# Performance work log

Hardware: AMD Instinct MI355X
Metric: run time of the kernel (lower is better)

Reference implementation:

```python
import jax, jax.numpy as jnp
import numpy as np

E, H, F, T = 8, 2048, 4096, 16384  # experts, hidden, ffn, total tokens


def setup_inputs() -> dict:
    key = jax.random.key(0)
    k1, k2, k3 = jax.random.split(key, 3)
    std = 1.0 / np.sqrt(H)
    x = jax.random.normal(k1, (T, H), dtype=jnp.float32)
    # trunc_normal_(std=std) ~ normal * std for reference purposes
    w_gate_up = jax.random.normal(k2, (E, 2 * F, H), dtype=jnp.float32) * std
    w_down = jax.random.normal(k3, (E, H, F), dtype=jnp.float32) * std
    # tokens are pre-sorted by expert; uniform routing: T//E tokens per expert
    tokens_per_expert = jnp.full((E,), T // E, dtype=jnp.int64)
    return {"x": x, "w_gate_up": w_gate_up, "w_down": w_down,
            "tokens_per_expert": tokens_per_expert}


def reference(x, w_gate_up, w_down, tokens_per_expert):
    # x: [T, H] sorted by expert; uniform tokens_per_expert => grouped GEMM
    # is a batched GEMM over the expert axis (same math as the per-expert
    # sequential fallback: gate_up = xi @ w_gate_up[i].T, etc.).
    e = w_gate_up.shape[0]
    f = w_down.shape[2]
    xe = x.reshape(e, -1, x.shape[-1])                     # [E, T/E, H]
    gate_up = jnp.einsum('eth,efh->etf', xe, w_gate_up)    # [E, T/E, 2F]
    gate, up = gate_up[..., :f], gate_up[..., f:]
    hidden = jax.nn.silu(gate) * up                        # [E, T/E, F]
    out = jnp.einsum('etf,ehf->eth', hidden, w_down)       # [E, T/E, H]
    return out.reshape(x.shape)
```

## Files before the change

kernel.cpp:

```cpp
#include <hip/hip_runtime.h>
#include <stdint.h>

typedef unsigned short u16;
typedef unsigned int u32;
typedef short bf16x8 __attribute__((ext_vector_type(8)));
typedef float f32x4 __attribute__((ext_vector_type(4)));

#define E_ 8
#define H_ 2048
#define F_ 4096
#define T_ 16384
#define TE_ 2048

#define WAITV(n) asm volatile("s_waitcnt vmcnt(" #n ")" ::: "memory")
#define BARF                       \
  do {                             \
    asm volatile("" ::: "memory"); \
    __builtin_amdgcn_s_barrier();  \
    asm volatile("" ::: "memory"); \
  } while (0)

__device__ __forceinline__ u16 f2bf(float f) {
  u32 u = __builtin_bit_cast(u32, f);
  u32 r = (u + 0x7FFFu + ((u >> 16) & 1u)) >> 16;
  return (u16)r;
}

__device__ __forceinline__ void gload16(const u16* g, u16* l) {
  __builtin_amdgcn_global_load_lds(
      (__attribute__((address_space(1))) void*)g,
      (__attribute__((address_space(3))) void*)l, 16, 0, 0);
}

__device__ __forceinline__ void mfma_b(f32x4& acc, bf16x8 a, bf16x8 b) {
  asm volatile("v_mfma_f32_16x16x32_bf16 %0, %1, %2, %0"
               : "+v"(acc)
               : "v"(a), "v"(b));
}


__global__ __launch_bounds__(256) void cvt_kernel(const float* __restrict__ src,
                                                  u16* __restrict__ dst,
                                                  long n4) {
  long i = (long)blockIdx.x * blockDim.x + threadIdx.x;
  long stride = (long)gridDim.x * blockDim.x;
  const float4* s4 = (const float4*)src;
  uint2* d4 = (uint2*)dst;
  for (; i < n4; i += stride) {
    float4 v = s4[i];
    uint2 o;
    o.x = (u32)f2bf(v.x) | ((u32)f2bf(v.y) << 16);
    o.y = (u32)f2bf(v.z) | ((u32)f2bf(v.w) << 16);
    d4[i] = o;
  }
}


__global__ __launch_bounds__(256, 2) void gemm1_silu(
    const u16* __restrict__ Xb, const u16* __restrict__ Wgu,
    u16* __restrict__ Hid, long sX, long sW, long sH) {
  const int z = blockIdx.z;
  Xb += (long)z * sX;
  Wgu += (long)z * sW;
  Hid += (long)z * sH;

  const int bx = blockIdx.x;
  const int by = blockIdx.y;
  const int tid = threadIdx.x;
  const int w = tid >> 6;
  const int lane = tid & 63;
  const int wr = w >> 1, wc = w & 1;
  const int fr = lane & 15, q = lane >> 4, l7 = lane & 7;

  __shared__ __attribute__((aligned(16))) u16 lds[2 * 16384];

  const int srow8 = lane >> 3;
  const int sgran = (lane & 7) ^ (lane >> 3);
  const u16* gA = Xb + (size_t)(by * 128 + srow8) * H_ + sgran * 8;
  const u16* gBg = Wgu + (size_t)(bx * 64 + srow8) * H_ + sgran * 8;
  const u16* gBu = gBg + (size_t)F_ * H_;

  auto stage = [&](int t, int buf) {
    u16* L = lds + buf * 16384;
    const int ko = t * 64;
#pragma unroll
    for (int i = 0; i < 4; ++i) {
      const int c = i * 4 + w;
      gload16(gA + (size_t)(c * 8) * H_ + ko, L + c * 512 + lane * 8);
    }
#pragma unroll
    for (int i = 0; i < 2; ++i) {
      const int c = i * 4 + w;
      gload16(gBg + (size_t)(c * 8) * H_ + ko, L + 8192 + c * 512 + lane * 8);
      gload16(gBu + (size_t)(c * 8) * H_ + ko, L + 12288 + c * 512 + lane * 8);
    }
  };

  f32x4 accG[4][2] = {};
  f32x4 accU[4][2] = {};

  auto comp = [&](int buf) {
    const u16* L = lds + buf * 16384;
#pragma unroll
    for (int ks = 0; ks < 2; ++ks) {
      const int seg = (((ks << 2) + q) ^ l7) << 3;
      bf16x8 a[4], bg[2], bu[2];
#pragma unroll
      for (int mi = 0; mi < 4; ++mi)
        a[mi] = *(const bf16x8*)&L[(wr * 64 + mi * 16 + fr) * 64 + seg];
#pragma unroll
      for (int ni = 0; ni < 2; ++ni) {
        bg[ni] = *(const bf16x8*)&L[8192 + (wc * 32 + ni * 16 + fr) * 64 + seg];
        bu[ni] =
            *(const bf16x8*)&L[12288 + (wc * 32 + ni * 16 + fr) * 64 + seg];
      }
      __builtin_amdgcn_s_setprio(1);
#pragma unroll
      for (int mi = 0; mi < 4; ++mi)
#pragma unroll
        for (int ni = 0; ni < 2; ++ni) {
          mfma_b(accG[mi][ni], a[mi], bg[ni]);
          mfma_b(accU[mi][ni], a[mi], bu[ni]);
        }
      __builtin_amdgcn_s_setprio(0);
    }
  };

  const int NT = H_ / 64;
  stage(0, 0);
  stage(1, 1);
  for (int t = 0; t < NT - 1; ++t) {
    WAITV(8);
    BARF;
    comp(t & 1);
    BARF;
    if (t + 2 < NT) stage(t + 2, t & 1);
  }
  WAITV(0);
  BARF;
  comp((NT - 1) & 1);

  const int row0 = by * 128 + wr * 64 + q * 4;
  const int col0 = bx * 64 + wc * 32 + fr;
#pragma unroll
  for (int mi = 0; mi < 4; ++mi)
#pragma unroll
    for (int ni = 0; ni < 2; ++ni)
#pragma unroll
      for (int j = 0; j < 4; ++j) {
        float g = accG[mi][ni][j];
        float u = accU[mi][ni][j];
        float h = (g / (1.f + __expf(-g))) * u;
        Hid[(size_t)(row0 + mi * 16 + j) * F_ + col0 + ni * 16] = f2bf(h);
      }
}


__global__ __launch_bounds__(256, 2) void gemm2_down(
    const u16* __restrict__ Hd, const u16* __restrict__ Wd,
    float* __restrict__ Out, long sH, long sW, long sO) {
  const int z = blockIdx.z;
  Hd += (long)z * sH;
  Wd += (long)z * sW;
  Out += (long)z * sO;

  const int bx = blockIdx.x;
  const int by = blockIdx.y;
  const int tid = threadIdx.x;
  const int w = tid >> 6;
  const int lane = tid & 63;
  const int wr = w >> 1, wc = w & 1;
  const int fr = lane & 15, q = lane >> 4, l7 = lane & 7;

  __shared__ __attribute__((aligned(16))) u16 lds[2 * 16384];

  const int srow8 = lane >> 3;
  const int sgran = (lane & 7) ^ (lane >> 3);
  const u16* gA = Hd + (size_t)(by * 128 + srow8) * F_ + sgran * 8;
  const u16* gB = Wd + (size_t)(bx * 128 + srow8) * F_ + sgran * 8;

  auto stage = [&](int t, int buf) {
    u16* L = lds + buf * 16384;
    const int ko = t * 64;
#pragma unroll
    for (int i = 0; i < 4; ++i) {
      const int c = i * 4 + w;
      gload16(gA + (size_t)(c * 8) * F_ + ko, L + c * 512 + lane * 8);
      gload16(gB + (size_t)(c * 8) * F_ + ko, L + 8192 + c * 512 + lane * 8);
    }
  };

  f32x4 acc[4][4] = {};

  auto comp = [&](int buf) {
    const u16* L = lds + buf * 16384;
#pragma unroll
    for (int ks = 0; ks < 2; ++ks) {
      const int seg = (((ks << 2) + q) ^ l7) << 3;
      bf16x8 a[4], b[4];
#pragma unroll
      for (int mi = 0; mi < 4; ++mi)
        a[mi] = *(const bf16x8*)&L[(wr * 64 + mi * 16 + fr) * 64 + seg];
#pragma unroll
      for (int ni = 0; ni < 4; ++ni)
        b[ni] = *(const bf16x8*)&L[8192 + (wc * 64 + ni * 16 + fr) * 64 + seg];
      __builtin_amdgcn_s_setprio(1);
#pragma unroll
      for (int mi = 0; mi < 4; ++mi)
#pragma unroll
        for (int ni = 0; ni < 4; ++ni) mfma_b(acc[mi][ni], a[mi], b[ni]);
      __builtin_amdgcn_s_setprio(0);
    }
  };

  const int NT = F_ / 64;
  stage(0, 0);
  stage(1, 1);
  for (int t = 0; t < NT - 1; ++t) {
    WAITV(8);
    BARF;
    comp(t & 1);
    BARF;
    if (t + 2 < NT) stage(t + 2, t & 1);
  }
  WAITV(0);
  BARF;
  comp((NT - 1) & 1);

  const int row0 = by * 128 + wr * 64 + q * 4;
  const int col0 = bx * 128 + wc * 64 + fr;
#pragma unroll
  for (int mi = 0; mi < 4; ++mi)
#pragma unroll
    for (int ni = 0; ni < 4; ++ni)
#pragma unroll
      for (int j = 0; j < 4; ++j)
        Out[(size_t)(row0 + mi * 16 + j) * H_ + col0 + ni * 16] =
            acc[mi][ni][j];
}


extern "C" void kernel_launch(void* const* d_in, const int* in_sizes, int n_in,
                              void* d_out, int out_size, void* d_ws,
                              size_t ws_size, hipStream_t stream) {
  (void)in_sizes;
  (void)n_in;
  (void)out_size;
  const float* x = (const float*)d_in[0];
  const float* wgu = (const float*)d_in[1];
  const float* wdn = (const float*)d_in[2];
  float* out = (float*)d_out;
  u16* ws = (u16*)d_ws;

  const size_t xbN = (size_t)T_ * H_;
  const size_t wguN = (size_t)E_ * 2 * F_ * H_;
  const size_t wdnN = (size_t)E_ * H_ * F_;
  const size_t hidN = (size_t)T_ * F_;
  const size_t fullBytes = (xbN + wguN + wdnN + hidN) * 2;

  dim3 cblk(256), gblk(256);

  if (ws_size >= fullBytes) {
    u16* xb = ws;
    u16* wgub = xb + xbN;
    u16* wdnb = wgub + wguN;
    u16* hid = wdnb + wdnN;
    cvt_kernel<<<2048, cblk, 0, stream>>>(x, xb, (long)(xbN / 4));
    cvt_kernel<<<4096, cblk, 0, stream>>>(wgu, wgub, (long)(wguN / 4));
    cvt_kernel<<<4096, cblk, 0, stream>>>(wdn, wdnb, (long)(wdnN / 4));
    gemm1_silu<<<dim3(F_ / 64, TE_ / 128, E_), gblk, 0, stream>>>(
        xb, wgub, hid, (long)TE_ * H_, (long)2 * F_ * H_, (long)TE_ * F_);
    gemm2_down<<<dim3(H_ / 128, TE_ / 128, E_), gblk, 0, stream>>>(
        hid, wdnb, out, (long)TE_ * F_, (long)H_ * F_, (long)TE_ * H_);
  } else {
    u16* xb = ws;
    u16* wgub = xb + (size_t)TE_ * H_;
    u16* wdnb = wgub + (size_t)2 * F_ * H_;
    u16* hid = wdnb + (size_t)H_ * F_;
    for (int e = 0; e < E_; ++e) {
      cvt_kernel<<<1024, cblk, 0, stream>>>(x + (size_t)e * TE_ * H_, xb,
                                            (long)((size_t)TE_ * H_ / 4));
      cvt_kernel<<<2048, cblk, 0, stream>>>(wgu + (size_t)e * 2 * F_ * H_, wgub,
                                            (long)((size_t)2 * F_ * H_ / 4));
      cvt_kernel<<<2048, cblk, 0, stream>>>(wdn + (size_t)e * H_ * F_, wdnb,
                                            (long)((size_t)H_ * F_ / 4));
      gemm1_silu<<<dim3(F_ / 64, TE_ / 128, 1), gblk, 0, stream>>>(xb, wgub,
                                                                   hid, 0, 0,
                                                                   0);
      gemm2_down<<<dim3(H_ / 128, TE_ / 128, 1), gblk, 0, stream>>>(
          hid, wdnb, out + (size_t)e * TE_ * H_, 0, 0, 0);
    }
  }
}
```

Before: 1.075 ms.

## Merge x/w_gate_up conversions and overlap w_down conversion with gemm1

Replaces the two separate fp32-to-bf16 conversion launches for x and w_gate_up with one launch that splits its blocks between the two arrays. It also adds an extra column of blocks to the gemm1 grid that converts w_down while the GEMM blocks run, which removes the standalone w_down conversion launch. The aim is to cut launch overhead and tail gaps and to hide the w_down conversion behind gemm1's compute. The risk is that the conversion blocks compete with the GEMM for bandwidth and CU slots. In the fallback path the conversion blocks are indexed only by blockIdx.y, so the fixed 131072-element chunk size must match each expert's w_down slice for the conversion to be complete and stay in bounds.

Result: slower. 1.286 ms (+19.6%).

```diff
diff --git a/kernel.cpp b/kernel.cpp
--- a/kernel.cpp
+++ b/kernel.cpp
@@ -38,33 +38,55 @@
                : "v"(a), "v"(b));
 }
 
-
-__global__ __launch_bounds__(256) void cvt_kernel(const float* __restrict__ src,
-                                                  u16* __restrict__ dst,
-                                                  long n4) {
-  long i = (long)blockIdx.x * blockDim.x + threadIdx.x;
-  long stride = (long)gridDim.x * blockDim.x;
-  const float4* s4 = (const float4*)src;
-  uint2* d4 = (uint2*)dst;
-  for (; i < n4; i += stride) {
-    float4 v = s4[i];
-    uint2 o;
-    o.x = (u32)f2bf(v.x) | ((u32)f2bf(v.y) << 16);
-    o.y = (u32)f2bf(v.z) | ((u32)f2bf(v.w) << 16);
-    d4[i] = o;
+__device__ __forceinline__ void cvt_f4(const float4* __restrict__ s4,
+                                       uint2* __restrict__ d4, long i) {
+  float4 v = s4[i];
+  uint2 o;
+  o.x = (u32)f2bf(v.x) | ((u32)f2bf(v.y) << 16);
+  o.y = (u32)f2bf(v.z) | ((u32)f2bf(v.w) << 16);
+  d4[i] = o;
+}
+
+
+__global__ __launch_bounds__(256) void cvt2_kernel(
+    const float* __restrict__ s0, u16* __restrict__ d0, long n0,
+    const float* __restrict__ s1, u16* __restrict__ d1, long n1, int b0) {
+  if ((int)blockIdx.x < b0) {
+    long i = (long)blockIdx.x * blockDim.x + threadIdx.x;
+    long stride = (long)b0 * blockDim.x;
+    const float4* s4 = (const float4*)s0;
+    uint2* d4 = (uint2*)d0;
+    for (; i < n0; i += stride) cvt_f4(s4, d4, i);
+  } else {
+    long i = (long)(blockIdx.x - b0) * blockDim.x + threadIdx.x;
+    long stride = (long)(gridDim.x - b0) * blockDim.x;
+    const float4* s4 = (const float4*)s1;
+    uint2* d4 = (uint2*)d1;
+    for (; i < n1; i += stride) cvt_f4(s4, d4, i);
   }
 }
 
 
 __global__ __launch_bounds__(256, 2) void gemm1_silu(
     const u16* __restrict__ Xb, const u16* __restrict__ Wgu,
-    u16* __restrict__ Hid, long sX, long sW, long sH) {
+    u16* __restrict__ Hid, const float* __restrict__ WdnSrc,
+    u16* __restrict__ WdnDst, long sX, long sW, long sH) {
+  const int bx = blockIdx.x;
+  if (bx == (int)gridDim.x - 1) {
+    const long cid = (long)blockIdx.z * gridDim.y + blockIdx.y;
+    const long base = cid * 131072;
+    const float4* s4 = (const float4*)WdnSrc;
+    uint2* d4 = (uint2*)WdnDst;
+    for (long i = base + threadIdx.x; i < base + 131072; i += 256)
+      cvt_f4(s4, d4, i);
+    return;
+  }
+
   const int z = blockIdx.z;
   Xb += (long)z * sX;
   Wgu += (long)z * sW;
   Hid += (long)z * sH;
 
-  const int bx = blockIdx.x;
   const int by = blockIdx.y;
   const int tid = threadIdx.x;
   const int w = tid >> 6;
@@ -265,11 +287,11 @@
     u16* wgub = xb + xbN;
     u16* wdnb = wgub + wguN;
     u16* hid = wdnb + wdnN;
-    cvt_kernel<<<2048, cblk, 0, stream>>>(x, xb, (long)(xbN / 4));
-    cvt_kernel<<<4096, cblk, 0, stream>>>(wgu, wgub, (long)(wguN / 4));
-    cvt_kernel<<<4096, cblk, 0, stream>>>(wdn, wdnb, (long)(wdnN / 4));
-    gemm1_silu<<<dim3(F_ / 64, TE_ / 128, E_), gblk, 0, stream>>>(
-        xb, wgub, hid, (long)TE_ * H_, (long)2 * F_ * H_, (long)TE_ * F_);
+    cvt2_kernel<<<4096, cblk, 0, stream>>>(x, xb, (long)(xbN / 4), wgu, wgub,
+                                           (long)(wguN / 4), 832);
+    gemm1_silu<<<dim3(F_ / 64 + 1, TE_ / 128, E_), gblk, 0, stream>>>(
+        xb, wgub, hid, wdn, wdnb, (long)TE_ * H_, (long)2 * F_ * H_,
+        (long)TE_ * F_);
     gemm2_down<<<dim3(H_ / 128, TE_ / 128, E_), gblk, 0, stream>>>(
         hid, wdnb, out, (long)TE_ * F_, (long)H_ * F_, (long)TE_ * H_);
   } else {
@@ -278,15 +300,12 @@
     u16* wdnb = wgub + (size_t)2 * F_ * H_;
     u16* hid = wdnb + (size_t)H_ * F_;
     for (int e = 0; e < E_; ++e) {
-      cvt_kernel<<<1024, cblk, 0, stream>>>(x + (size_t)e * TE_ * H_, xb,
-                                            (long)((size_t)TE_ * H_ / 4));
-      cvt_kernel<<<2048, cblk, 0, stream>>>(wgu + (size_t)e * 2 * F_ * H_, wgub,
-                                            (long)((size_t)2 * F_ * H_ / 4));
-      cvt_kernel<<<2048, cblk, 0, stream>>>(wdn + (size_t)e * H_ * F_, wdnb,
-                                            (long)((size_t)H_ * F_ / 4));
-      gemm1_silu<<<dim3(F_ / 64, TE_ / 128, 1), gblk, 0, stream>>>(xb, wgub,
-                                                                   hid, 0, 0,
-                                                                   0);
+      cvt2_kernel<<<2048, cblk, 0, stream>>>(
+          x + (size_t)e * TE_ * H_, xb, (long)((size_t)TE_ * H_ / 4),
+          wgu + (size_t)e * 2 * F_ * H_, wgub,
+          (long)((size_t)2 * F_ * H_ / 4), 410);
+      gemm1_silu<<<dim3(F_ / 64 + 1, TE_ / 128, 1), gblk, 0, stream>>>(
+          xb, wgub, hid, wdn + (size_t)e * H_ * F_, wdnb, 0, 0, 0);
       gemm2_down<<<dim3(H_ / 128, TE_ / 128, 1), gblk, 0, stream>>>(
           hid, wdnb, out + (size_t)e * TE_ * H_, 0, 0, 0);
     }
```

## Fuse fp32 weight-to-bf16 conversion into GEMM B-tile staging

Applied to the files above, without the earlier changes.

Removes the standalone weight conversion kernels. The GEMMs now load fp32 weights into registers, convert them with packed bf16 conversion instructions and store them to LDS, using a register-staged double-buffer pipeline. This cuts a full extra read/write pass over the large weight tensors. In exchange, each block re-reads twice as many bytes for its weight tiles and uses more registers for staging, which may lower occupancy.

New measurement: 1.331 ms. 23.8% more time.

```diff
diff --git a/kernel.cpp b/kernel.cpp
--- a/kernel.cpp
+++ b/kernel.cpp
@@ -13,6 +13,7 @@
 #define TE_ 2048
 
 #define WAITV(n) asm volatile("s_waitcnt vmcnt(" #n ")" ::: "memory")
+#define LGKM0 asm volatile("s_waitcnt lgkmcnt(0)" ::: "memory")
 #define BARF                       \
   do {                             \
     asm volatile("" ::: "memory"); \
@@ -24,6 +25,12 @@
   u32 u = __builtin_bit_cast(u32, f);
   u32 r = (u + 0x7FFFu + ((u >> 16) & 1u)) >> 16;
   return (u16)r;
+}
+
+__device__ __forceinline__ u32 cvtpk(float lo, float hi) {
+  u32 r;
+  asm("v_cvt_pk_bf16_f32 %0, %1, %2" : "=v"(r) : "v"(lo), "v"(hi));
+  return r;
 }
 
 __device__ __forceinline__ void gload16(const u16* g, u16* l) {
@@ -57,7 +64,7 @@
 
 
 __global__ __launch_bounds__(256, 2) void gemm1_silu(
-    const u16* __restrict__ Xb, const u16* __restrict__ Wgu,
+    const u16* __restrict__ Xb, const float* __restrict__ Wgu,
     u16* __restrict__ Hid, long sX, long sW, long sH) {
   const int z = blockIdx.z;
   Xb += (long)z * sX;
@@ -77,10 +84,10 @@
   const int srow8 = lane >> 3;
   const int sgran = (lane & 7) ^ (lane >> 3);
   const u16* gA = Xb + (size_t)(by * 128 + srow8) * H_ + sgran * 8;
-  const u16* gBg = Wgu + (size_t)(bx * 64 + srow8) * H_ + sgran * 8;
-  const u16* gBu = gBg + (size_t)F_ * H_;
-
-  auto stage = [&](int t, int buf) {
+  const float4* gB4 =
+      (const float4*)Wgu + (size_t)(bx * 64 + srow8) * (H_ / 4) + sgran * 2;
+
+  auto stageA = [&](int t, int buf) {
     u16* L = lds + buf * 16384;
     const int ko = t * 64;
 #pragma unroll
@@ -88,11 +95,32 @@
       const int c = i * 4 + w;
       gload16(gA + (size_t)(c * 8) * H_ + ko, L + c * 512 + lane * 8);
     }
-#pragma unroll
-    for (int i = 0; i < 2; ++i) {
-      const int c = i * 4 + w;
-      gload16(gBg + (size_t)(c * 8) * H_ + ko, L + 8192 + c * 512 + lane * 8);
-      gload16(gBu + (size_t)(c * 8) * H_ + ko, L + 12288 + c * 512 + lane * 8);
+  };
+
+  auto loadB = [&](float4* r, int t) {
+    const size_t kt = (size_t)t * 16;
+#pragma unroll
+    for (int i = 0; i < 4; ++i) {
+      const int c = i * 4 + w;
+      const size_t roff = (i < 2) ? (size_t)c * 8 * (H_ / 4)
+                                  : (size_t)F_ * (H_ / 4) +
+                                        (size_t)(c - 8) * 8 * (H_ / 4);
+      r[2 * i] = gB4[roff + kt];
+      r[2 * i + 1] = gB4[roff + kt + 1];
+    }
+  };
+
+  auto writeB = [&](int buf, const float4* r) {
+    u16* L = lds + buf * 16384;
+#pragma unroll
+    for (int i = 0; i < 4; ++i) {
+      const int c = i * 4 + w;
+      uint4 v;
+      v.x = cvtpk(r[2 * i].x, r[2 * i].y);
+      v.y = cvtpk(r[2 * i].z, r[2 * i].w);
+      v.z = cvtpk(r[2 * i + 1].x, r[2 * i + 1].y);
+      v.w = cvtpk(r[2 * i + 1].z, r[2 * i + 1].w);
+      *(uint4*)&L[8192 + c * 512 + lane * 8] = v;
     }
   };
 
@@ -126,19 +154,45 @@
     }
   };
 
+  float4 rB0[8], rB1[8];
   const int NT = H_ / 64;
-  stage(0, 0);
-  stage(1, 1);
-  for (int t = 0; t < NT - 1; ++t) {
-    WAITV(8);
-    BARF;
-    comp(t & 1);
-    BARF;
-    if (t + 2 < NT) stage(t + 2, t & 1);
+  loadB(rB0, 0);
+  stageA(0, 0);
+  loadB(rB1, 1);
+  stageA(1, 1);
+  WAITV(16);
+  writeB(0, rB0);
+  WAITV(12);
+  LGKM0;
+  BARF;
+  for (int t = 0; t < NT - 2; t += 2) {
+    comp(0);
+    BARF;
+    loadB(rB0, t + 2);
+    stageA(t + 2, 0);
+    WAITV(16);
+    writeB(1, rB1);
+    WAITV(12);
+    LGKM0;
+    BARF;
+    comp(1);
+    BARF;
+    loadB(rB1, t + 3);
+    stageA(t + 3, 1);
+    WAITV(16);
+    writeB(0, rB0);
+    WAITV(12);
+    LGKM0;
+    BARF;
   }
+  comp(0);
+  BARF;
+  WAITV(4);
+  writeB(1, rB1);
   WAITV(0);
-  BARF;
-  comp((NT - 1) & 1);
+  LGKM0;
+  BARF;
+  comp(1);
 
   const int row0 = by * 128 + wr * 64 + q * 4;
   const int col0 = bx * 64 + wc * 32 + fr;
@@ -157,7 +211,7 @@
 
 
 __global__ __launch_bounds__(256, 2) void gemm2_down(
-    const u16* __restrict__ Hd, const u16* __restrict__ Wd,
+    const u16* __restrict__ Hd, const float* __restrict__ Wd,
     float* __restrict__ Out, long sH, long sW, long sO) {
   const int z = blockIdx.z;
   Hd += (long)z * sH;
@@ -177,16 +231,41 @@
   const int srow8 = lane >> 3;
   const int sgran = (lane & 7) ^ (lane >> 3);
   const u16* gA = Hd + (size_t)(by * 128 + srow8) * F_ + sgran * 8;
-  const u16* gB = Wd + (size_t)(bx * 128 + srow8) * F_ + sgran * 8;
-
-  auto stage = [&](int t, int buf) {
+  const float4* gB4 =
+      (const float4*)Wd + (size_t)(bx * 128 + srow8) * (F_ / 4) + sgran * 2;
+
+  auto stageA = [&](int t, int buf) {
     u16* L = lds + buf * 16384;
     const int ko = t * 64;
 #pragma unroll
     for (int i = 0; i < 4; ++i) {
       const int c = i * 4 + w;
       gload16(gA + (size_t)(c * 8) * F_ + ko, L + c * 512 + lane * 8);
-      gload16(gB + (size_t)(c * 8) * F_ + ko, L + 8192 + c * 512 + lane * 8);
+    }
+  };
+
+  auto loadB = [&](float4* r, int t) {
+    const size_t kt = (size_t)t * 16;
+#pragma unroll
+    for (int i = 0; i < 4; ++i) {
+      const int c = i * 4 + w;
+      const size_t roff = (size_t)c * 8 * (F_ / 4);
+      r[2 * i] = gB4[roff + kt];
+      r[2 * i + 1] = gB4[roff + kt + 1];
+    }
+  };
+
+  auto writeB = [&](int buf, const float4* r) {
+    u16* L = lds + buf * 16384;
+#pragma unroll
+    for (int i = 0; i < 4; ++i) {
+      const int c = i * 4 + w;
+      uint4 v;
+      v.x = cvtpk(r[2 * i].x, r[2 * i].y);
+      v.y = cvtpk(r[2 * i].z, r[2 * i].w);
+      v.z = cvtpk(r[2 * i + 1].x, r[2 * i + 1].y);
+      v.w = cvtpk(r[2 * i + 1].z, r[2 * i + 1].w);
+      *(uint4*)&L[8192 + c * 512 + lane * 8] = v;
     }
   };
 
@@ -213,19 +292,45 @@
     }
   };
 
+  float4 rB0[8], rB1[8];
   const int NT = F_ / 64;
-  stage(0, 0);
-  stage(1, 1);
-  for (int t = 0; t < NT - 1; ++t) {
-    WAITV(8);
-    BARF;
-    comp(t & 1);
-    BARF;
-    if (t + 2 < NT) stage(t + 2, t & 1);
+  loadB(rB0, 0);
+  stageA(0, 0);
+  loadB(rB1, 1);
+  stageA(1, 1);
+  WAITV(16);
+  writeB(0, rB0);
+  WAITV(12);
+  LGKM0;
+  BARF;
+  for (int t = 0; t < NT - 2; t += 2) {
+    comp(0);
+    BARF;
+    loadB(rB0, t + 2);
+    stageA(t + 2, 0);
+    WAITV(16);
+    writeB(1, rB1);
+    WAITV(12);
+    LGKM0;
+    BARF;
+    comp(1);
+    BARF;
+    loadB(rB1, t + 3);
+    stageA(t + 3, 1);
+    WAITV(16);
+    writeB(0, rB0);
+    WAITV(12);
+    LGKM0;
+    BARF;
   }
+  comp(0);
+  BARF;
+  WAITV(4);
+  writeB(1, rB1);
   WAITV(0);
-  BARF;
-  comp((NT - 1) & 1);
+  LGKM0;
+  BARF;
+  comp(1);
 
   const int row0 = by * 128 + wr * 64 + q * 4;
   const int col0 = bx * 128 + wc * 64 + fr;
@@ -253,42 +358,29 @@
   u16* ws = (u16*)d_ws;
 
   const size_t xbN = (size_t)T_ * H_;
-  const size_t wguN = (size_t)E_ * 2 * F_ * H_;
-  const size_t wdnN = (size_t)E_ * H_ * F_;
   const size_t hidN = (size_t)T_ * F_;
-  const size_t fullBytes = (xbN + wguN + wdnN + hidN) * 2;
+  const size_t fullBytes = (xbN + hidN) * 2;
 
   dim3 cblk(256), gblk(256);
 
   if (ws_size >= fullBytes) {
     u16* xb = ws;
-    u16* wgub = xb + xbN;
-    u16* wdnb = wgub + wguN;
-    u16* hid = wdnb + wdnN;
-    cvt_kernel<<<2048, cblk, 0, stream>>>(x, xb, (long)(xbN / 4));
-    cvt_kernel<<<4096, cblk, 0, stream>>>(wgu, wgub, (long)(wguN / 4));
-    cvt_kernel<<<4096, cblk, 0, stream>>>(wdn, wdnb, (long)(wdnN / 4));
+    u16* hid = xb + xbN;
+    cvt_kernel<<<1024, cblk, 0, stream>>>(x, xb, (long)(xbN / 4));
     gemm1_silu<<<dim3(F_ / 64, TE_ / 128, E_), gblk, 0, stream>>>(
-        xb, wgub, hid, (long)TE_ * H_, (long)2 * F_ * H_, (long)TE_ * F_);
+        xb, wgu, hid, (long)TE_ * H_, (long)2 * F_ * H_, (long)TE_ * F_);
     gemm2_down<<<dim3(H_ / 128, TE_ / 128, E_), gblk, 0, stream>>>(
-        hid, wdnb, out, (long)TE_ * F_, (long)H_ * F_, (long)TE_ * H_);
+        hid, wdn, out, (long)TE_ * F_, (long)H_ * F_, (long)TE_ * H_);
   } else {
     u16* xb = ws;
-    u16* wgub = xb + (size_t)TE_ * H_;
-    u16* wdnb = wgub + (size_t)2 * F_ * H_;
-    u16* hid = wdnb + (size_t)H_ * F_;
+    u16* hid = xb + (size_t)TE_ * H_;
     for (int e = 0; e < E_; ++e) {
-      cvt_kernel<<<1024, cblk, 0, stream>>>(x + (size_t)e * TE_ * H_, xb,
-                                            (long)((size_t)TE_ * H_ / 4));
-      cvt_kernel<<<2048, cblk, 0, stream>>>(wgu + (size_t)e * 2 * F_ * H_, wgub,
-                                            (long)((size_t)2 * F_ * H_ / 4));
-      cvt_kernel<<<2048, cblk, 0, stream>>>(wdn + (size_t)e * H_ * F_, wdnb,
-                                            (long)((size_t)H_ * F_ / 4));
-      gemm1_silu<<<dim3(F_ / 64, TE_ / 128, 1), gblk, 0, stream>>>(xb, wgub,
-                                                                   hid, 0, 0,
-                                                                   0);
+      cvt_kernel<<<512, cblk, 0, stream>>>(x + (size_t)e * TE_ * H_, xb,
+                                           (long)((size_t)TE_ * H_ / 4));
+      gemm1_silu<<<dim3(F_ / 64, TE_ / 128, 1), gblk, 0, stream>>>(
+          xb, wgu + (size_t)e * 2 * F_ * H_, hid, 0, 0, 0);
       gemm2_down<<<dim3(H_ / 128, TE_ / 128, 1), gblk, 0, stream>>>(
-          hid, wdnb, out + (size_t)e * TE_ * H_, 0, 0, 0);
+          hid, wdn + (size_t)e * H_ * F_, out + (size_t)e * TE_ * H_, 0, 0, 0);
     }
   }
 }
```
